# Kernel tuning notes

Hardware: AMD Instinct MI355X
Metric: run time of the kernel (lower is better)

## Reference

```python
import jax, jax.numpy as jnp
import numpy as np

NUM_QUERIES = 300

B, S, NUM_LABELS, D = 32, 8400, 80, 256


def setup_inputs() -> dict:
    key = jax.random.key(0)
    k1, k2, k3, k4 = jax.random.split(key, 4)
    return {
        "enc_outputs_class": jax.random.normal(k1, (B, S, NUM_LABELS), dtype=jnp.float32),
        "enc_outputs_coord": jax.random.normal(k2, (B, S, 4), dtype=jnp.float32),
        "output_memory": jax.random.normal(k3, (B, S, D), dtype=jnp.float32),
        "sources_last_element": jax.random.normal(k4, (B, 400, D), dtype=jnp.float32),
    }


def reference(enc_outputs_class, enc_outputs_coord, output_memory, sources_last_element):
    # Per-token confidence: max over class logits. [B, S]
    scores = jnp.max(enc_outputs_class, axis=-1)
    # Top-k token indices per batch element (sorted=True as in keras.ops.top_k).
    _, topk_ind = jax.lax.top_k(scores, NUM_QUERIES)  # [B, K]
    idx = topk_ind[:, :, None]  # [B, K, 1], broadcasts over feature dim

    # Batched gathers (vectorized replacement for keras.ops.map + take).
    reference_points_unact = jnp.take_along_axis(enc_outputs_coord, idx, axis=1)  # [B, K, 4]
    enc_topk_logits = jnp.take_along_axis(enc_outputs_class, idx, axis=1)  # [B, K, NUM_LABELS]
    enc_topk_bboxes = jax.nn.sigmoid(reference_points_unact)  # [B, K, 4]

    # learn_initial_query=False path: gather decoder targets from encoder memory.
    target = jax.lax.stop_gradient(jnp.take_along_axis(output_memory, idx, axis=1))  # [B, K, D]

    init_reference_points = jax.lax.stop_gradient(reference_points_unact)
    return (init_reference_points, target, enc_topk_logits, enc_topk_bboxes)
```

## Files before the change

### kernel.cpp

```cpp
#include <hip/hip_runtime.h>
#include <stdint.h>

#define BB 32
#define SS 8400
#define LL 80
#define DD 256
#define KK 300

__device__ __forceinline__ uint32_t f32_desc_ord(float f) {
    uint32_t u = __builtin_bit_cast(uint32_t, f);
    uint32_t asc = (u & 0x80000000u) ? ~u : (u | 0x80000000u);
    return ~asc;
}

__global__ __launch_bounds__(256) void k_scores(const float* __restrict__ cls,
                                                uint32_t* __restrict__ keys32) {
    int r = blockIdx.x * 256 + threadIdx.x;
    const float4* row = (const float4*)(cls + (size_t)r * LL);
    float m = -3.4e38f;
#pragma unroll
    for (int i = 0; i < 20; ++i) {
        float4 v = row[i];
        m = fmaxf(m, fmaxf(fmaxf(v.x, v.y), fmaxf(v.z, v.w)));
    }
    keys32[r] = f32_desc_ord(m);
}

__global__ __launch_bounds__(1024) void k_topk(const uint32_t* __restrict__ keys32,
                                               int* __restrict__ topk) {
    __shared__ uint32_t keys[SS];
    __shared__ uint32_t hist[256];
    __shared__ uint32_t wsum[4];
    __shared__ unsigned long long sel[512];
    __shared__ uint32_t sh_prefix, sh_k, sh_cnt;

    const int b = blockIdx.x;
    const int tid = threadIdx.x;
    const int lane = tid & 63;
    const uint32_t* src = keys32 + (size_t)b * SS;

    for (int i = tid; i < SS; i += 1024) keys[i] = src[i];
    if (tid == 0) { sh_prefix = 0u; sh_k = KK; sh_cnt = 0u; }
    __syncthreads();

    for (int pos = 24; pos >= 0; pos -= 8) {
        if (tid < 256) hist[tid] = 0u;
        const uint32_t pref = sh_prefix;
        const uint32_t krem = sh_k;
        __syncthreads();

#pragma unroll
        for (int r = 0; r < 9; ++r) {
            int i = tid + r * 1024;
            uint32_t d = 256u;
            if (i < SS) {
                uint32_t key = keys[i];
                if (pos == 24 || (key >> (pos + 8)) == pref)
                    d = (key >> pos) & 0xFFu;
            }
            unsigned long long mask = ~0ull;
#pragma unroll
            for (int bit = 0; bit < 9; ++bit) {
                unsigned long long bb = __ballot((d >> bit) & 1u);
                mask &= ((d >> bit) & 1u) ? bb : ~bb;
            }
            if (d < 256u && (int)__builtin_ctzll(mask) == lane)
                atomicAdd(&hist[d], (uint32_t)__popcll(mask));
        }
        __syncthreads();

        uint32_t h = 0u, cwave = 0u;
        if (tid < 256) {
            h = hist[tid];
            cwave = h;
#pragma unroll
            for (int off = 1; off < 64; off <<= 1) {
                uint32_t n = __shfl_up(cwave, (unsigned)off, 64);
                if (lane >= off) cwave += n;
            }
            if (lane == 63) wsum[tid >> 6] = cwave;
        }
        __syncthreads();
        if (tid < 256) {
            uint32_t base = 0u;
            for (int w = 0; w < (tid >> 6); ++w) base += wsum[w];
            uint32_t cumInc = base + cwave;
            uint32_t cumExc = cumInc - h;
            if (cumExc < krem && krem <= cumInc) {
                sh_prefix = (pref << 8) | (uint32_t)tid;
                sh_k = krem - cumExc;
            }
        }
        __syncthreads();
    }

    const uint32_t T = sh_prefix;
    for (int i = tid; i < SS; i += 1024) {
        uint32_t key = keys[i];
        if (key <= T) {
            uint32_t p = atomicAdd(&sh_cnt, 1u);
            if (p < 512u) sel[p] = ((unsigned long long)key << 32) | (uint32_t)i;
        }
    }
    __syncthreads();

    uint32_t cnt = sh_cnt < 512u ? sh_cnt : 512u;
    if (tid < (int)cnt) {
        unsigned long long mine = sel[tid];
        uint32_t rank = 0u;
        for (uint32_t m = 0; m < cnt; ++m) rank += (sel[m] < mine) ? 1u : 0u;
        if (rank < KK) topk[b * KK + rank] = (int)(uint32_t)(mine & 0xFFFFFFFFull);
    }
}

__global__ __launch_bounds__(64) void k_gather(const float* __restrict__ coord,
                                               const float* __restrict__ cls,
                                               const float* __restrict__ mem,
                                               const int* __restrict__ topk,
                                               float* __restrict__ out) {
    const int r = blockIdx.x;
    const int b = r / KK;
    const int t = threadIdx.x;
    const int idx = topk[r];
    const size_t srow = (size_t)b * SS + (size_t)idx;

    const size_t O1 = (size_t)BB * KK * 4;
    const size_t O2 = O1 + (size_t)BB * KK * DD;
    const size_t O3 = O2 + (size_t)BB * KK * LL;

    {
        const float4* s = (const float4*)(mem + srow * DD);
        float4* d = (float4*)(out + O1 + (size_t)r * DD);
        d[t] = s[t];
    }
    if (t < 20) {
        const float4* s = (const float4*)(cls + srow * LL);
        float4* d = (float4*)(out + O2 + (size_t)r * LL);
        d[t] = s[t];
    }
    if (t == 0) {
        float4 v = *(const float4*)(coord + srow * 4);
        *(float4*)(out + (size_t)r * 4) = v;
        float4 o;
        o.x = 1.0f / (1.0f + expf(-v.x));
        o.y = 1.0f / (1.0f + expf(-v.y));
        o.z = 1.0f / (1.0f + expf(-v.z));
        o.w = 1.0f / (1.0f + expf(-v.w));
        *(float4*)(out + O3 + (size_t)r * 4) = o;
    }
}

extern "C" void kernel_launch(void* const* d_in, const int* in_sizes, int n_in,
                              void* d_out, int out_size, void* d_ws, size_t ws_size,
                              hipStream_t stream) {
    const float* cls   = (const float*)d_in[0];
    const float* coord = (const float*)d_in[1];
    const float* mem   = (const float*)d_in[2];
    float* out = (float*)d_out;

    uint32_t* keys32 = (uint32_t*)d_ws;
    int* topk = (int*)((char*)d_ws + (size_t)BB * SS * 4);

    k_scores<<<(BB * SS) / 256, 256, 0, stream>>>(cls, keys32);
    k_topk<<<BB, 1024, 0, stream>>>(keys32, topk);
    k_gather<<<BB * KK, 64, 0, stream>>>(coord, cls, mem, topk, out);
}
```

Measured before the change: 408.8 us.

## Coalesce score reduction and compact candidate lists in radix top-k select

The score kernel now has each block read 64 rows with coalesced float4 loads across threads and reduce per-row maxima through shared-memory atomicMax on order-preserving keys, replacing strided per-thread row reads. The top-k kernel builds the first histogram while loading keys, then after each radix pass compacts surviving candidate indices into shrinking 16-bit lists via wave-aggregated appends. Later passes scan only those lists instead of all 8400 keys, and histograms are replicated four ways to reduce atomic contention. This adds shared-memory usage and fixed list capacities.

```diff
diff --git a/kernel.cpp b/kernel.cpp
--- a/kernel.cpp
+++ b/kernel.cpp
@@ -7,99 +7,154 @@
 #define DD 256
 #define KK 300
 
-__device__ __forceinline__ uint32_t f32_desc_ord(float f) {
-    uint32_t u = __builtin_bit_cast(uint32_t, f);
-    uint32_t asc = (u & 0x80000000u) ? ~u : (u | 0x80000000u);
-    return ~asc;
-}
-
 __global__ __launch_bounds__(256) void k_scores(const float* __restrict__ cls,
                                                 uint32_t* __restrict__ keys32) {
-    int r = blockIdx.x * 256 + threadIdx.x;
-    const float4* row = (const float4*)(cls + (size_t)r * LL);
-    float m = -3.4e38f;
+    __shared__ uint32_t smax[64];
+    const int tid = threadIdx.x;
+    const size_t rowBase = (size_t)blockIdx.x * 64;
+    const float4* src = (const float4*)(cls + rowBase * LL);
+    if (tid < 64) smax[tid] = 0u;
+    __syncthreads();
 #pragma unroll
-    for (int i = 0; i < 20; ++i) {
-        float4 v = row[i];
-        m = fmaxf(m, fmaxf(fmaxf(v.x, v.y), fmaxf(v.z, v.w)));
-    }
-    keys32[r] = f32_desc_ord(m);
+    for (int j = 0; j < 5; ++j) {
+        int fi = j * 256 + tid;
+        float4 v = src[fi];
+        float m = fmaxf(fmaxf(v.x, v.y), fmaxf(v.z, v.w));
+        uint32_t u = __builtin_bit_cast(uint32_t, m);
+        uint32_t asc = (u & 0x80000000u) ? ~u : (u | 0x80000000u);
+        atomicMax(&smax[fi / 20], asc);
+    }
+    __syncthreads();
+    if (tid < 64) keys32[rowBase + tid] = ~smax[tid];
+}
+
+__device__ __forceinline__ void wave_append_u16(bool cond, uint16_t val, int lane,
+                                                uint32_t* counter, uint16_t* list,
+                                                uint32_t cap) {
+    unsigned long long m = __ballot(cond);
+    if (m != 0ull) {
+        int leader = (int)__builtin_ctzll(m);
+        uint32_t base = 0;
+        if (lane == leader) base = atomicAdd(counter, (uint32_t)__popcll(m));
+        base = (uint32_t)__shfl((int)base, leader, 64);
+        if (cond) {
+            uint32_t p = base + (uint32_t)__popcll(m & ((1ull << lane) - 1ull));
+            if (p < cap) list[p] = val;
+        }
+    }
 }
 
 __global__ __launch_bounds__(1024) void k_topk(const uint32_t* __restrict__ keys32,
                                                int* __restrict__ topk) {
     __shared__ uint32_t keys[SS];
-    __shared__ uint32_t hist[256];
+    __shared__ uint16_t listA[SS];
+    __shared__ uint16_t listB[2048];
+    __shared__ uint32_t hist[4 * 260];
+    __shared__ unsigned long long sel[512];
     __shared__ uint32_t wsum[4];
-    __shared__ unsigned long long sel[512];
-    __shared__ uint32_t sh_prefix, sh_k, sh_cnt;
+    __shared__ uint32_t sh_prefix, sh_k, sh_cnt, sh_nA, sh_nB;
 
     const int b = blockIdx.x;
     const int tid = threadIdx.x;
     const int lane = tid & 63;
+    const int rep = (tid >> 7) & 3;
     const uint32_t* src = keys32 + (size_t)b * SS;
 
-    for (int i = tid; i < SS; i += 1024) keys[i] = src[i];
-    if (tid == 0) { sh_prefix = 0u; sh_k = KK; sh_cnt = 0u; }
-    __syncthreads();
-
-    for (int pos = 24; pos >= 0; pos -= 8) {
-        if (tid < 256) hist[tid] = 0u;
-        const uint32_t pref = sh_prefix;
-        const uint32_t krem = sh_k;
-        __syncthreads();
-
-#pragma unroll
-        for (int r = 0; r < 9; ++r) {
-            int i = tid + r * 1024;
-            uint32_t d = 256u;
-            if (i < SS) {
-                uint32_t key = keys[i];
-                if (pos == 24 || (key >> (pos + 8)) == pref)
-                    d = (key >> pos) & 0xFFu;
-            }
-            unsigned long long mask = ~0ull;
-#pragma unroll
-            for (int bit = 0; bit < 9; ++bit) {
-                unsigned long long bb = __ballot((d >> bit) & 1u);
-                mask &= ((d >> bit) & 1u) ? bb : ~bb;
-            }
-            if (d < 256u && (int)__builtin_ctzll(mask) == lane)
-                atomicAdd(&hist[d], (uint32_t)__popcll(mask));
-        }
-        __syncthreads();
-
-        uint32_t h = 0u, cwave = 0u;
-        if (tid < 256) {
-            h = hist[tid];
-            cwave = h;
-#pragma unroll
-            for (int off = 1; off < 64; off <<= 1) {
-                uint32_t n = __shfl_up(cwave, (unsigned)off, 64);
-                if (lane >= off) cwave += n;
-            }
-            if (lane == 63) wsum[tid >> 6] = cwave;
-        }
-        __syncthreads();
-        if (tid < 256) {
-            uint32_t base = 0u;
-            for (int w = 0; w < (tid >> 6); ++w) base += wsum[w];
-            uint32_t cumInc = base + cwave;
-            uint32_t cumExc = cumInc - h;
-            if (cumExc < krem && krem <= cumInc) {
-                sh_prefix = (pref << 8) | (uint32_t)tid;
-                sh_k = krem - cumExc;
-            }
-        }
-        __syncthreads();
-    }
-
-    const uint32_t T = sh_prefix;
+    if (tid == 0) { sh_prefix = 0u; sh_k = KK; sh_cnt = 0u; sh_nA = 0u; sh_nB = 0u; }
+
+#define SCAN_SELECT()                                                          \
+    {                                                                          \
+        uint32_t krem = sh_k, pref = sh_prefix;                                \
+        uint32_t h = 0, cwave = 0;                                             \
+        if (tid < 256) {                                                       \
+            h = hist[tid] + hist[260 + tid] + hist[520 + tid] + hist[780 + tid]; \
+            cwave = h;                                                         \
+            _Pragma("unroll")                                                  \
+            for (int off = 1; off < 64; off <<= 1) {                           \
+                uint32_t nv = __shfl_up(cwave, (unsigned)off, 64);             \
+                if (lane >= off) cwave += nv;                                  \
+            }                                                                  \
+            if (lane == 63) wsum[tid >> 6] = cwave;                            \
+        }                                                                      \
+        __syncthreads();          \
+        if (tid < 256) {                                                       \
+            uint32_t base = 0;                                                 \
+            for (int w = 0; w < (tid >> 6); ++w) base += wsum[w];              \
+            uint32_t cumInc = base + cwave, cumExc = cumInc - h;               \
+            if (cumExc < krem && krem <= cumInc) {        \
+                sh_prefix = (pref << 8) | (uint32_t)tid;                       \
+                sh_k = krem - cumExc;                                          \
+            }                                                                  \
+        }                                                                      \
+        __syncthreads();                                                       \
+    }
+
+#define ZERO_HIST()                                                            \
+    for (int i = tid; i < 4 * 260; i += 1024) hist[i] = 0u;
+
+    ZERO_HIST();
+    __syncthreads();
+    for (int i = tid; i < SS; i += 1024) {
+        uint32_t key = src[i];
+        keys[i] = key;
+        atomicAdd(&hist[rep * 260 + (key >> 24)], 1u);
+    }
+    __syncthreads();
+    SCAN_SELECT();
+
+    ZERO_HIST();
+    const uint32_t d1 = sh_prefix;
+    __syncthreads();
     for (int i = tid; i < SS; i += 1024) {
         uint32_t key = keys[i];
-        if (key <= T) {
-            uint32_t p = atomicAdd(&sh_cnt, 1u);
-            if (p < 512u) sel[p] = ((unsigned long long)key << 32) | (uint32_t)i;
+        uint32_t b3 = key >> 24;
+        if (b3 == d1) atomicAdd(&hist[rep * 260 + ((key >> 16) & 0xFFu)], 1u);
+        wave_append_u16(b3 <= d1, (uint16_t)i, lane, &sh_nA, listA, SS);
+    }
+    __syncthreads();
+    SCAN_SELECT();
+
+    ZERO_HIST();
+    const uint32_t p16 = sh_prefix;
+    const int nA = (int)sh_nA;
+    __syncthreads();
+    for (int j = tid; j < nA; j += 1024) {
+        uint16_t idx = listA[j];
+        uint32_t key = keys[idx];
+        uint32_t t16 = key >> 16;
+        if (t16 == p16) atomicAdd(&hist[rep * 260 + ((key >> 8) & 0xFFu)], 1u);
+        wave_append_u16(t16 <= p16, idx, lane, &sh_nB, listB, 2048u);
+    }
+    __syncthreads();
+    SCAN_SELECT();
+
+    ZERO_HIST();
+    const uint32_t p24 = sh_prefix;
+    int nB = (int)sh_nB;
+    if (nB > 2048) nB = 2048;
+    __syncthreads();
+    for (int j = tid; j < nB; j += 1024) {
+        uint32_t key = keys[listB[j]];
+        if ((key >> 8) == p24) atomicAdd(&hist[rep * 260 + (key & 0xFFu)], 1u);
+    }
+    __syncthreads();
+    SCAN_SELECT();
+
+    const uint32_t T = sh_prefix;
+    for (int j = tid; j < nB; j += 1024) {
+        uint16_t idx = listB[j];
+        uint32_t key = keys[idx];
+        bool cond = key <= T;
+        unsigned long long m = __ballot(cond);
+        if (m != 0ull) {
+            int leader = (int)__builtin_ctzll(m);
+            uint32_t base = 0;
+            if (lane == leader) base = atomicAdd(&sh_cnt, (uint32_t)__popcll(m));
+            base = (uint32_t)__shfl((int)base, leader, 64);
+            if (cond) {
+                uint32_t p = base + (uint32_t)__popcll(m & ((1ull << lane) - 1ull));
+                if (p < 512u) sel[p] = ((unsigned long long)key << 32) | idx;
+            }
         }
     }
     __syncthreads();
@@ -108,9 +163,11 @@
     if (tid < (int)cnt) {
         unsigned long long mine = sel[tid];
         uint32_t rank = 0u;
-        for (uint32_t m = 0; m < cnt; ++m) rank += (sel[m] < mine) ? 1u : 0u;
+        for (uint32_t m2 = 0; m2 < cnt; ++m2) rank += (sel[m2] < mine) ? 1u : 0u;
         if (rank < KK) topk[b * KK + rank] = (int)(uint32_t)(mine & 0xFFFFFFFFull);
     }
+#undef SCAN_SELECT
+#undef ZERO_HIST
 }
 
 __global__ __launch_bounds__(64) void k_gather(const float* __restrict__ coord,
@@ -161,7 +218,7 @@
     uint32_t* keys32 = (uint32_t*)d_ws;
     int* topk = (int*)((char*)d_ws + (size_t)BB * SS * 4);
 
-    k_scores<<<(BB * SS) / 256, 256, 0, stream>>>(cls, keys32);
+    k_scores<<<(BB * SS) / 64, 256, 0, stream>>>(cls, keys32);
     k_topk<<<BB, 1024, 0, stream>>>(keys32, topk);
     k_gather<<<BB * KK, 64, 0, stream>>>(coord, cls, mem, topk, out);
 }
```

Result: faster. 392.8 us (-3.9%).

## Single-pass 13-bit radix select for top-k and coalesce score reduction

Applied to the files above, without the earlier changes.

The four-pass 8-bit radix select becomes a single 13-bit histogram pass over keys read straight from global memory. A block-wide scan then finds the threshold bucket, and survivors are compacted with warp-aggregated atomics into a 1024-entry candidate buffer that is rank-sorted. The score kernel now loads class logits with coalesced float4 reads, stores partial maxima in shared memory and reduces them per row. The aim is fewer synchronised histogram passes in the 32-block top-k kernel and better memory coalescing in the score kernel. The cost is a larger candidate set (up to 1024) with quadratic ranking, and a correctness risk if the threshold bucket holds too many keys.

```diff
diff --git a/kernel.cpp b/kernel.cpp
--- a/kernel.cpp
+++ b/kernel.cpp
@@ -7,108 +7,124 @@
 #define DD 256
 #define KK 300
 
-__device__ __forceinline__ uint32_t f32_desc_ord(float f) {
-    uint32_t u = __builtin_bit_cast(uint32_t, f);
-    uint32_t asc = (u & 0x80000000u) ? ~u : (u | 0x80000000u);
-    return ~asc;
-}
-
 __global__ __launch_bounds__(256) void k_scores(const float* __restrict__ cls,
                                                 uint32_t* __restrict__ keys32) {
-    int r = blockIdx.x * 256 + threadIdx.x;
-    const float4* row = (const float4*)(cls + (size_t)r * LL);
-    float m = -3.4e38f;
+    __shared__ float sval[64 * 21];
+    const int tid = threadIdx.x;
+    const size_t rowBase = (size_t)blockIdx.x * 64;
+    const float4* src = (const float4*)(cls + rowBase * LL);
 #pragma unroll
-    for (int i = 0; i < 20; ++i) {
-        float4 v = row[i];
-        m = fmaxf(m, fmaxf(fmaxf(v.x, v.y), fmaxf(v.z, v.w)));
+    for (int j = 0; j < 5; ++j) {
+        int fi = j * 256 + tid;
+        float4 v = src[fi];
+        int r = fi / 20, c = fi - r * 20;
+        sval[r * 21 + c] = fmaxf(fmaxf(v.x, v.y), fmaxf(v.z, v.w));
     }
-    keys32[r] = f32_desc_ord(m);
+    __syncthreads();
+    if (tid < 64) {
+        const float* row = &sval[tid * 21];
+        float m = row[0];
+#pragma unroll
+        for (int i = 1; i < 20; ++i) m = fmaxf(m, row[i]);
+        uint32_t u = __builtin_bit_cast(uint32_t, m);
+        uint32_t asc = (u & 0x80000000u) ? ~u : (u | 0x80000000u);
+        keys32[rowBase + tid] = ~asc;
+    }
 }
 
 __global__ __launch_bounds__(1024) void k_topk(const uint32_t* __restrict__ keys32,
                                                int* __restrict__ topk) {
-    __shared__ uint32_t keys[SS];
-    __shared__ uint32_t hist[256];
-    __shared__ uint32_t wsum[4];
-    __shared__ unsigned long long sel[512];
-    __shared__ uint32_t sh_prefix, sh_k, sh_cnt;
+    __shared__ uint32_t hist[8192];
+    __shared__ unsigned long long sel[1024];
+    __shared__ uint32_t wtot[16];
+    __shared__ uint32_t sh_p, sh_cnt;
 
     const int b = blockIdx.x;
     const int tid = threadIdx.x;
     const int lane = tid & 63;
+    const int wid = tid >> 6;
     const uint32_t* src = keys32 + (size_t)b * SS;
 
-    for (int i = tid; i < SS; i += 1024) keys[i] = src[i];
-    if (tid == 0) { sh_prefix = 0u; sh_k = KK; sh_cnt = 0u; }
+    for (int i = tid; i < 8192; i += 1024) hist[i] = 0u;
+    if (tid == 0) { sh_p = 0u; sh_cnt = 0u; }
     __syncthreads();
 
-    for (int pos = 24; pos >= 0; pos -= 8) {
-        if (tid < 256) hist[tid] = 0u;
-        const uint32_t pref = sh_prefix;
-        const uint32_t krem = sh_k;
-        __syncthreads();
+#pragma unroll
+    for (int r = 0; r < 9; ++r) {
+        int i = tid + r * 1024;
+        uint32_t d = 16383u;
+        if (i < SS) d = src[i] >> 19;
+        unsigned long long mask = ~0ull;
+#pragma unroll
+        for (int bit = 0; bit < 14; ++bit) {
+            unsigned long long bb = __ballot((d >> bit) & 1u);
+            mask &= ((d >> bit) & 1u) ? bb : ~bb;
+        }
+        if (d < 8192u && (int)__builtin_ctzll(mask) == lane)
+            atomicAdd(&hist[d], (uint32_t)__popcll(mask));
+    }
+    __syncthreads();
 
+    uint32_t loc[8];
+    uint32_t s = 0;
 #pragma unroll
-        for (int r = 0; r < 9; ++r) {
-            int i = tid + r * 1024;
-            uint32_t d = 256u;
-            if (i < SS) {
-                uint32_t key = keys[i];
-                if (pos == 24 || (key >> (pos + 8)) == pref)
-                    d = (key >> pos) & 0xFFu;
-            }
-            unsigned long long mask = ~0ull;
+    for (int i = 0; i < 8; ++i) { loc[i] = hist[8 * tid + i]; s += loc[i]; }
+    uint32_t w = s;
 #pragma unroll
-            for (int bit = 0; bit < 9; ++bit) {
-                unsigned long long bb = __ballot((d >> bit) & 1u);
-                mask &= ((d >> bit) & 1u) ? bb : ~bb;
-            }
-            if (d < 256u && (int)__builtin_ctzll(mask) == lane)
-                atomicAdd(&hist[d], (uint32_t)__popcll(mask));
+    for (int off = 1; off < 64; off <<= 1) {
+        uint32_t n = __shfl_up(w, (unsigned)off, 64);
+        if (lane >= off) w += n;
+    }
+    if (lane == 63) wtot[wid] = w;
+    __syncthreads();
+    if (tid < 16) {
+        uint32_t v = wtot[tid];
+#pragma unroll
+        for (int off = 1; off < 16; off <<= 1) {
+            uint32_t n = __shfl_up(v, (unsigned)off, 64);
+            if (lane >= off) v += n;
         }
-        __syncthreads();
-
-        uint32_t h = 0u, cwave = 0u;
-        if (tid < 256) {
-            h = hist[tid];
-            cwave = h;
+        wtot[tid] = v;
+    }
+    __syncthreads();
+    {
+        uint32_t base = (wid > 0) ? wtot[wid - 1] : 0u;
+        uint32_t cumInc = base + w;
+        uint32_t cumExc = cumInc - s;
+        if (cumExc < KK && KK <= cumInc) {
+            uint32_t c = cumExc;
 #pragma unroll
-            for (int off = 1; off < 64; off <<= 1) {
-                uint32_t n = __shfl_up(cwave, (unsigned)off, 64);
-                if (lane >= off) cwave += n;
-            }
-            if (lane == 63) wsum[tid >> 6] = cwave;
-        }
-        __syncthreads();
-        if (tid < 256) {
-            uint32_t base = 0u;
-            for (int w = 0; w < (tid >> 6); ++w) base += wsum[w];
-            uint32_t cumInc = base + cwave;
-            uint32_t cumExc = cumInc - h;
-            if (cumExc < krem && krem <= cumInc) {
-                sh_prefix = (pref << 8) | (uint32_t)tid;
-                sh_k = krem - cumExc;
+            for (int i = 0; i < 8; ++i) {
+                if (KK <= c + loc[i]) { sh_p = 8u * tid + i; break; }
+                c += loc[i];
             }
         }
-        __syncthreads();
     }
+    __syncthreads();
+    const uint32_t p13 = sh_p;
 
-    const uint32_t T = sh_prefix;
     for (int i = tid; i < SS; i += 1024) {
-        uint32_t key = keys[i];
-        if (key <= T) {
-            uint32_t p = atomicAdd(&sh_cnt, 1u);
-            if (p < 512u) sel[p] = ((unsigned long long)key << 32) | (uint32_t)i;
+        uint32_t key = src[i];
+        bool cond = (key >> 19) <= p13;
+        unsigned long long m = __ballot(cond);
+        if (m != 0ull) {
+            int leader = (int)__builtin_ctzll(m);
+            uint32_t base2 = 0;
+            if (lane == leader) base2 = atomicAdd(&sh_cnt, (uint32_t)__popcll(m));
+            base2 = (uint32_t)__shfl((int)base2, leader, 64);
+            if (cond) {
+                uint32_t p = base2 + (uint32_t)__popcll(m & ((1ull << lane) - 1ull));
+                if (p < 1024u) sel[p] = ((unsigned long long)key << 32) | (uint32_t)i;
+            }
         }
     }
     __syncthreads();
 
-    uint32_t cnt = sh_cnt < 512u ? sh_cnt : 512u;
+    uint32_t cnt = sh_cnt < 1024u ? sh_cnt : 1024u;
     if (tid < (int)cnt) {
         unsigned long long mine = sel[tid];
         uint32_t rank = 0u;
-        for (uint32_t m = 0; m < cnt; ++m) rank += (sel[m] < mine) ? 1u : 0u;
+        for (uint32_t m2 = 0; m2 < cnt; ++m2) rank += (sel[m2] < mine) ? 1u : 0u;
         if (rank < KK) topk[b * KK + rank] = (int)(uint32_t)(mine & 0xFFFFFFFFull);
     }
 }
@@ -161,7 +177,7 @@
     uint32_t* keys32 = (uint32_t*)d_ws;
     int* topk = (int*)((char*)d_ws + (size_t)BB * SS * 4);
 
-    k_scores<<<(BB * SS) / 256, 256, 0, stream>>>(cls, keys32);
+    k_scores<<<(BB * SS) / 64, 256, 0, stream>>>(cls, keys32);
     k_topk<<<BB, 1024, 0, stream>>>(keys32, topk);
     k_gather<<<BB * KK, 64, 0, stream>>>(coord, cls, mem, topk, out);
 }
```

Result: faster. 390.4 us (-4.5%).
